# Kernel tuning notes

Measured on AMD Instinct MI355X. Metric: run time of the kernel, lower is better.

Reference implementation:

```python
import jax, jax.numpy as jnp
import numpy as np

B, T, C = 256, 2048, 64  # batch, max_seq_len, num_classes


def setup_inputs() -> dict:
    key = jax.random.key(0)
    k1, k2, k3, k4 = jax.random.split(key, 4)
    pad_x = jax.random.normal(k1, (B, T, C), dtype=jnp.float32)
    transitions = jax.random.uniform(k2, (C, C), dtype=jnp.float32)
    origination = jax.random.uniform(k3, (C,), dtype=jnp.float32)
    batch_sizes = jnp.sort(jax.random.randint(k4, (B,), 1, T + 1))
    # the torch implementation assumes features are zero-padded past the length
    mask = jnp.arange(T)[None, :] < batch_sizes[:, None]  # (B, T)
    pad_x = pad_x * mask[:, :, None]
    return {"pad_x": pad_x, "transitions": transitions,
            "origination": origination, "batch_sizes": batch_sizes}


def reference(pad_x, transitions, origination, batch_sizes):
    # Linear-chain CRF forward algorithm (faithful to torch _forward_algo,
    # including the final sum over classes rather than logsumexp).
    x_tbc = jnp.swapaxes(pad_x, 0, 1)  # (T, B, C)
    alpha0 = x_tbc[0] + origination[None, :]  # (B, C)

    def step(alpha_prev, x_t):
        # scores[b, j, k] = alpha_prev[b, k] + transitions[j, k]
        scores = alpha_prev[:, None, :] + transitions[None, :, :]  # (B, C, C)
        alpha = x_t + jax.nn.logsumexp(scores, axis=2)  # (B, C)
        return alpha, alpha

    _, alphas_rest = jax.lax.scan(step, alpha0, x_tbc[1:])
    alphas = jnp.concatenate([alpha0[None], alphas_rest], axis=0)  # (T, B, C)
    # gather alpha at the last valid timestep of each sequence
    final = alphas[batch_sizes - 1, jnp.arange(pad_x.shape[0])]  # (B, C)
    return final.sum(axis=1)  # (B,)
```

## Files before the change

### kernel.cpp

```cpp
#include <hip/hip_runtime.h>


#define CC 64

typedef short bf16x8 __attribute__((ext_vector_type(8)));
typedef float f32x4 __attribute__((ext_vector_type(4)));

union PackAB { int w[4]; bf16x8 v; };

__device__ __forceinline__ int cvtpk(float lo, float hi) {
    int r;
    asm("v_cvt_pk_bf16_f32 %0, %1, %2" : "=v"(r) : "v"(lo), "v"(hi));
    return r;
}
__device__ __forceinline__ float bcast0(float v) {
    return __int_as_float(__builtin_amdgcn_readfirstlane(__float_as_int(v)));
}

#define LDS_FENCE() asm volatile("s_waitcnt lgkmcnt(0)" ::: "memory")

template <bool SCALE>
__device__ __forceinline__ void chain_step(const bf16x8 (&A)[4][2], PackAB (&Bf)[2][4],
                                           const f32x4* __restrict__ er4, int g,
                                           float r_, float& ns0) {
    f32x4 er[4];
    #pragma unroll
    for (int mt = 0; mt < 4; ++mt) {
        er[mt] = er4[4 * mt + g];
        if (SCALE) er[mt] *= r_;
    }

    f32x4 D[4][4];
    #pragma unroll
    for (int nt = 0; nt < 4; ++nt) {
        f32x4 Z = {0.f, 0.f, 0.f, 0.f};
        #pragma unroll
        for (int mt = 0; mt < 4; ++mt)
            D[nt][mt] = __builtin_amdgcn_mfma_f32_16x16x32_bf16(A[mt][0], Bf[0][nt].v, Z, 0, 0, 0);
    }
    #pragma unroll
    for (int nt = 0; nt < 4; ++nt)
        #pragma unroll
        for (int mt = 0; mt < 4; ++mt)
            D[nt][mt] = __builtin_amdgcn_mfma_f32_16x16x32_bf16(A[mt][1], Bf[1][nt].v, D[nt][mt], 0, 0, 0);

    ns0 = D[0][0][0];

    #pragma unroll
    for (int nt = 0; nt < 4; ++nt) {
        f32x4 d0 = D[nt][0] * er[0];
        f32x4 d1 = D[nt][1] * er[1];
        f32x4 d2 = D[nt][2] * er[2];
        f32x4 d3 = D[nt][3] * er[3];
        Bf[0][nt].w[0] = cvtpk(d0[0], d0[1]);
        Bf[0][nt].w[1] = cvtpk(d0[2], d0[3]);
        Bf[0][nt].w[2] = cvtpk(d1[0], d1[1]);
        Bf[0][nt].w[3] = cvtpk(d1[2], d1[3]);
        Bf[1][nt].w[0] = cvtpk(d2[0], d2[1]);
        Bf[1][nt].w[1] = cvtpk(d2[2], d2[3]);
        Bf[1][nt].w[2] = cvtpk(d3[0], d3[1]);
        Bf[1][nt].w[3] = cvtpk(d3[2], d3[3]);
    }

    __builtin_amdgcn_sched_group_barrier(0x100, 4, 0);
    __builtin_amdgcn_sched_group_barrier(0x008, 32, 0);
    __builtin_amdgcn_sched_group_barrier(0x002, 80, 0);
}

__launch_bounds__(64, 2)
__global__ void crf_seg_kernel(const float* __restrict__ x,
                               const float* __restrict__ trans,
                               const int*   __restrict__ lens,
                               unsigned short* __restrict__ Mws,
                               float* __restrict__ Ls,
                               int T, int Pseg, int SEG, int B) {
    const int blk = blockIdx.x;
    const int b = B - 1 - (blk >> 6);
    const int s = blk & (Pseg - 1);
    const int L = lens[b];
    const int tbeg = s * SEG;
    int segend = (s + 1) * SEG; if (segend > L - 1) segend = L - 1;
    const int nsteps = segend - tbeg;
    if (nsteps <= 0) return;

    const int l = threadIdx.x;
    const int c = l & 15, g = l >> 4;
    const float L2E = 1.4426950408889634f;
    const float* xb = x + (size_t)b * T * CC;

    __shared__ float xl[32][CC];

    {
        const int rl = l >> 4;
        const int cl = (l & 15) * 4;
        f32x4 st[8];
        #pragma unroll
        for (int i = 0; i < 8; ++i) {
            int tr = tbeg + 1 + 4 * i + rl;
            if (tr > segend) tr = segend;
            st[i] = *(const f32x4*)(xb + (size_t)tr * CC + cl);
        }
        #pragma unroll
        for (int i = 0; i < 8; ++i) {
            f32x4 e;
            #pragma unroll
            for (int r = 0; r < 4; ++r)
                e[r] = __builtin_amdgcn_exp2f(st[i][r] * L2E);
            *(f32x4*)&xl[4 * i + rl][cl] = e;
        }
        LDS_FENCE();
    }

    bf16x8 A[4][2];
    #pragma unroll
    for (int mt = 0; mt < 4; ++mt) {
        const float* tr = trans + (16 * mt + c) * CC;
        #pragma unroll
        for (int ch = 0; ch < 2; ++ch) {
            float4 u = *(const float4*)(tr + 32 * ch + 4 * g);
            float4 v = *(const float4*)(tr + 32 * ch + 16 + 4 * g);
            PackAB pk;
            pk.w[0] = cvtpk(__builtin_amdgcn_exp2f(u.x * L2E), __builtin_amdgcn_exp2f(u.y * L2E));
            pk.w[1] = cvtpk(__builtin_amdgcn_exp2f(u.z * L2E), __builtin_amdgcn_exp2f(u.w * L2E));
            pk.w[2] = cvtpk(__builtin_amdgcn_exp2f(v.x * L2E), __builtin_amdgcn_exp2f(v.y * L2E));
            pk.w[3] = cvtpk(__builtin_amdgcn_exp2f(v.z * L2E), __builtin_amdgcn_exp2f(v.w * L2E));
            A[mt][ch] = pk.v;
        }
    }
    PackAB Bf[2][4];
    #pragma unroll
    for (int ch = 0; ch < 2; ++ch)
        #pragma unroll
        for (int nt = 0; nt < 4; ++nt)
            #pragma unroll
            for (int qq = 0; qq < 4; ++qq) {
                int i0 = 2 * qq, i1 = 2 * qq + 1;
                int k0 = 32 * ch + 4 * g + (i0 & 3) + 16 * (i0 >> 2);
                int k1 = 32 * ch + 4 * g + (i1 & 3) + 16 * (i1 >> 2);
                Bf[ch][nt].w[qq] = cvtpk((k0 == 16 * nt + c) ? 1.f : 0.f,
                                         (k1 == 16 * nt + c) ? 1.f : 0.f);
            }

    float Lseg = 0.f, ns0 = 1.0f;
    for (int base = 0; base < nsteps; base += 4) {
        float r_ = 1.0f;
        if (base > 0) {
            float S00 = bcast0(ns0);
            r_ = __builtin_amdgcn_rcpf(S00);
            Lseg -= __builtin_amdgcn_logf(r_);
        }
        chain_step<true >(A, Bf, (const f32x4*)&xl[base][0], g, r_, ns0);
        if (base + 1 < nsteps) chain_step<false>(A, Bf, (const f32x4*)&xl[base + 1][0], g, 1.f, ns0);
        if (base + 2 < nsteps) chain_step<false>(A, Bf, (const f32x4*)&xl[base + 2][0], g, 1.f, ns0);
        if (base + 3 < nsteps) chain_step<false>(A, Bf, (const f32x4*)&xl[base + 3][0], g, 1.f, ns0);
    }

    unsigned short* Mo = Mws + ((size_t)b * Pseg + s) * 4096;
    #pragma unroll
    for (int ch = 0; ch < 2; ++ch)
        #pragma unroll
        for (int nt = 0; nt < 4; ++nt)
            #pragma unroll
            for (int e = 0; e < 8; ++e) {
                unsigned wb = (unsigned)Bf[ch][nt].w[e >> 1];
                unsigned short hb = (e & 1) ? (unsigned short)(wb >> 16)
                                            : (unsigned short)(wb & 0xffffu);
                int row = 32 * ch + 4 * g + (e & 3) + 16 * (e >> 2);
                Mo[row * 64 + 16 * nt + c] = hb;
            }
    if (l == 0) Ls[(size_t)b * Pseg + s] = Lseg;
}

__launch_bounds__(64, 1)
__global__ void crf_apply_kernel(const float* __restrict__ x,
                                 const float* __restrict__ orig,
                                 const int*   __restrict__ lens,
                                 const unsigned short* __restrict__ Mws,
                                 const float* __restrict__ Ls,
                                 float* __restrict__ out,
                                 int T, int Pseg, int SEG) {
    const int b = blockIdx.x, j = threadIdx.x;
    __shared__ float qb[CC];
    const float L2E = 1.4426950408889634f, LN2 = 0.6931471805599453f;
    const int L = lens[b];
    const float* xb = x + (size_t)b * T * CC;

    float Mbar = (xb[0] + orig[0]) * L2E;
    float q = __builtin_amdgcn_exp2f((xb[j] + orig[j]) * L2E - Mbar);

    uint4 R[8];
    {
        const uint4* Ms = (const uint4*)(Mws + ((size_t)b * Pseg + 0) * 4096 + j * 64);
        #pragma unroll
        for (int i = 0; i < 8; ++i) R[i] = Ms[i];
    }

    for (int s = 0; s < Pseg; ++s) {
        int tbeg = s * SEG;
        int segend = (s + 1) * SEG; if (segend > L - 1) segend = L - 1;
        if (segend - tbeg <= 0) break;

        uint4 Rc[8];
        #pragma unroll
        for (int i = 0; i < 8; ++i) Rc[i] = R[i];
        {
            int s2 = (s + 1 < Pseg) ? s + 1 : s;
            const uint4* Ms = (const uint4*)(Mws + ((size_t)b * Pseg + s2) * 4096 + j * 64);
            #pragma unroll
            for (int i = 0; i < 8; ++i) R[i] = Ms[i];
        }

        qb[j] = q;
        LDS_FENCE();

        float acc = 0.f;
        #pragma unroll
        for (int i = 0; i < 8; ++i) {
            f32x4 qv0 = *(const f32x4*)&qb[8 * i];
            f32x4 qv1 = *(const f32x4*)&qb[8 * i + 4];
            unsigned u0 = Rc[i].x, u1 = Rc[i].y, u2 = Rc[i].z, u3 = Rc[i].w;
            acc = fmaf(__uint_as_float(u0 << 16),        qv0[0], acc);
            acc = fmaf(__uint_as_float(u0 & 0xffff0000), qv0[1], acc);
            acc = fmaf(__uint_as_float(u1 << 16),        qv0[2], acc);
            acc = fmaf(__uint_as_float(u1 & 0xffff0000), qv0[3], acc);
            acc = fmaf(__uint_as_float(u2 << 16),        qv1[0], acc);
            acc = fmaf(__uint_as_float(u2 & 0xffff0000), qv1[1], acc);
            acc = fmaf(__uint_as_float(u3 << 16),        qv1[2], acc);
            acc = fmaf(__uint_as_float(u3 & 0xffff0000), qv1[3], acc);
        }
        float S = acc;
        Mbar += Ls[(size_t)b * Pseg + s];
        float p = bcast0(S);
        float r = __builtin_amdgcn_rcpf(p);
        float lgr = __builtin_amdgcn_logf(r);
        q = S * r;
        Mbar -= lgr;
        LDS_FENCE();
    }

    float alpha = LN2 * (Mbar + __builtin_amdgcn_logf(q));
    alpha += __shfl_xor(alpha, 1, 64);
    alpha += __shfl_xor(alpha, 2, 64);
    alpha += __shfl_xor(alpha, 4, 64);
    alpha += __shfl_xor(alpha, 8, 64);
    alpha += __shfl_xor(alpha, 16, 64);
    alpha += __shfl_xor(alpha, 32, 64);
    if (j == 0) out[b] = alpha;
}

extern "C" void kernel_launch(void* const* d_in, const int* in_sizes, int n_in,
                              void* d_out, int out_size, void* d_ws, size_t ws_size,
                              hipStream_t stream) {
    const float* x     = (const float*)d_in[0];
    const float* trans = (const float*)d_in[1];
    const float* orig  = (const float*)d_in[2];
    const int*   lens  = (const int*)d_in[3];
    float* out = (float*)d_out;

    const int B = in_sizes[3];
    const int T = in_sizes[0] / (B * CC);

    const int P = 64;
    const int SEG = (T + P - 1) / P;

    unsigned short* Mws = (unsigned short*)d_ws;
    float* Ls = (float*)(Mws + (size_t)B * P * 4096);

    crf_seg_kernel<<<B * P, 64, 0, stream>>>(x, trans, lens, Mws, Ls,
                                             T, P, SEG, B);
    crf_apply_kernel<<<B, 64, 0, stream>>>(x, orig, lens, Mws, Ls, out, T, P, SEG);
}
```

Before: 182.4 us.

## Split segment chain into two interleaved halves and merge via matrix product

Each wave's segment of transfer-matrix products is split into two independent 16-step sub-chains that run interleaved, giving the MFMA pipeline two independent dependency chains to overlap. The second half's product is staged through LDS, reloaded as an A operand, multiplied with the first half's result, then renormalized and packed back. This trades a longer serial MFMA dependency chain for extra registers, one more 64x64 matrix multiply, and an LDS round trip. It assumes the segment is at most 32 steps.

```diff
diff --git a/kernel.cpp b/kernel.cpp
--- a/kernel.cpp
+++ b/kernel.cpp
@@ -127,7 +127,7 @@
             A[mt][ch] = pk.v;
         }
     }
-    PackAB Bf[2][4];
+    PackAB Bf0[2][4], Bf1[2][4];
     #pragma unroll
     for (int ch = 0; ch < 2; ++ch)
         #pragma unroll
@@ -137,22 +137,99 @@
                 int i0 = 2 * qq, i1 = 2 * qq + 1;
                 int k0 = 32 * ch + 4 * g + (i0 & 3) + 16 * (i0 >> 2);
                 int k1 = 32 * ch + 4 * g + (i1 & 3) + 16 * (i1 >> 2);
-                Bf[ch][nt].w[qq] = cvtpk((k0 == 16 * nt + c) ? 1.f : 0.f,
-                                         (k1 == 16 * nt + c) ? 1.f : 0.f);
+                int idv = cvtpk((k0 == 16 * nt + c) ? 1.f : 0.f,
+                                (k1 == 16 * nt + c) ? 1.f : 0.f);
+                Bf0[ch][nt].w[qq] = idv;
+                Bf1[ch][nt].w[qq] = idv;
             }
 
-    float Lseg = 0.f, ns0 = 1.0f;
-    for (int base = 0; base < nsteps; base += 4) {
-        float r_ = 1.0f;
-        if (base > 0) {
-            float S00 = bcast0(ns0);
-            r_ = __builtin_amdgcn_rcpf(S00);
-            Lseg -= __builtin_amdgcn_logf(r_);
-        }
-        chain_step<true >(A, Bf, (const f32x4*)&xl[base][0], g, r_, ns0);
-        if (base + 1 < nsteps) chain_step<false>(A, Bf, (const f32x4*)&xl[base + 1][0], g, 1.f, ns0);
-        if (base + 2 < nsteps) chain_step<false>(A, Bf, (const f32x4*)&xl[base + 2][0], g, 1.f, ns0);
-        if (base + 3 < nsteps) chain_step<false>(A, Bf, (const f32x4*)&xl[base + 3][0], g, 1.f, ns0);
+    const int n0 = nsteps < 16 ? nsteps : 16;
+    int n1 = nsteps - 16; if (n1 < 0) n1 = 0;
+
+    float Ls0 = 0.f, ns00 = 1.0f;
+    float Ls1 = 0.f, ns01 = 1.0f;
+
+    for (int base = 0; base < 16; base += 4) {
+        float r0 = 1.0f, r1 = 1.0f;
+        if (base > 0 && base < n0) {
+            float S00 = bcast0(ns00);
+            r0 = __builtin_amdgcn_rcpf(S00);
+            Ls0 -= __builtin_amdgcn_logf(r0);
+        }
+        if (base > 0 && base < n1) {
+            float S01 = bcast0(ns01);
+            r1 = __builtin_amdgcn_rcpf(S01);
+            Ls1 -= __builtin_amdgcn_logf(r1);
+        }
+        if (base     < n0) chain_step<true >(A, Bf0, (const f32x4*)&xl[base][0],      g, r0,  ns00);
+        if (base     < n1) chain_step<true >(A, Bf1, (const f32x4*)&xl[16 + base][0], g, r1,  ns01);
+        if (base + 1 < n0) chain_step<false>(A, Bf0, (const f32x4*)&xl[base + 1][0],  g, 1.f, ns00);
+        if (base + 1 < n1) chain_step<false>(A, Bf1, (const f32x4*)&xl[16 + base + 1][0], g, 1.f, ns01);
+        if (base + 2 < n0) chain_step<false>(A, Bf0, (const f32x4*)&xl[base + 2][0],  g, 1.f, ns00);
+        if (base + 2 < n1) chain_step<false>(A, Bf1, (const f32x4*)&xl[16 + base + 2][0], g, 1.f, ns01);
+        if (base + 3 < n0) chain_step<false>(A, Bf0, (const f32x4*)&xl[base + 3][0],  g, 1.f, ns00);
+        if (base + 3 < n1) chain_step<false>(A, Bf1, (const f32x4*)&xl[16 + base + 3][0], g, 1.f, ns01);
+    }
+
+    float Lfinal = Ls0;
+    if (n1 > 0) {
+        unsigned short* Ml = (unsigned short*)&xl[0][0];
+        LDS_FENCE();
+        #pragma unroll
+        for (int ch = 0; ch < 2; ++ch)
+            #pragma unroll
+            for (int nt = 0; nt < 4; ++nt)
+                #pragma unroll
+                for (int e = 0; e < 8; ++e) {
+                    unsigned wb = (unsigned)Bf1[ch][nt].w[e >> 1];
+                    unsigned short hb = (e & 1) ? (unsigned short)(wb >> 16)
+                                                : (unsigned short)(wb & 0xffffu);
+                    int row = 32 * ch + 4 * g + (e & 3) + 16 * (e >> 2);
+                    Ml[row * 64 + 16 * nt + c] = hb;
+                }
+        LDS_FENCE();
+        bf16x8 Ah[4][2];
+        #pragma unroll
+        for (int mt = 0; mt < 4; ++mt)
+            #pragma unroll
+            for (int ch = 0; ch < 2; ++ch) {
+                PackAB pk;
+                *(uint2*)&pk.w[0] = *(const uint2*)(Ml + (16 * mt + c) * 64 + 32 * ch + 4 * g);
+                *(uint2*)&pk.w[2] = *(const uint2*)(Ml + (16 * mt + c) * 64 + 32 * ch + 16 + 4 * g);
+                Ah[mt][ch] = pk.v;
+            }
+        f32x4 D[4][4];
+        #pragma unroll
+        for (int nt = 0; nt < 4; ++nt) {
+            f32x4 Z = {0.f, 0.f, 0.f, 0.f};
+            #pragma unroll
+            for (int mt = 0; mt < 4; ++mt)
+                D[nt][mt] = __builtin_amdgcn_mfma_f32_16x16x32_bf16(Ah[mt][0], Bf0[0][nt].v, Z, 0, 0, 0);
+        }
+        #pragma unroll
+        for (int nt = 0; nt < 4; ++nt)
+            #pragma unroll
+            for (int mt = 0; mt < 4; ++mt)
+                D[nt][mt] = __builtin_amdgcn_mfma_f32_16x16x32_bf16(Ah[mt][1], Bf0[1][nt].v, D[nt][mt], 0, 0, 0);
+
+        float S00 = bcast0(D[0][0][0]);
+        float r_  = __builtin_amdgcn_rcpf(S00);
+        Lfinal = Ls0 + Ls1 - __builtin_amdgcn_logf(r_);
+        #pragma unroll
+        for (int nt = 0; nt < 4; ++nt) {
+            f32x4 d0 = D[nt][0] * r_;
+            f32x4 d1 = D[nt][1] * r_;
+            f32x4 d2 = D[nt][2] * r_;
+            f32x4 d3 = D[nt][3] * r_;
+            Bf0[0][nt].w[0] = cvtpk(d0[0], d0[1]);
+            Bf0[0][nt].w[1] = cvtpk(d0[2], d0[3]);
+            Bf0[0][nt].w[2] = cvtpk(d1[0], d1[1]);
+            Bf0[0][nt].w[3] = cvtpk(d1[2], d1[3]);
+            Bf0[1][nt].w[0] = cvtpk(d2[0], d2[1]);
+            Bf0[1][nt].w[1] = cvtpk(d2[2], d2[3]);
+            Bf0[1][nt].w[2] = cvtpk(d3[0], d3[1]);
+            Bf0[1][nt].w[3] = cvtpk(d3[2], d3[3]);
+        }
     }
 
     unsigned short* Mo = Mws + ((size_t)b * Pseg + s) * 4096;
@@ -162,13 +239,13 @@
         for (int nt = 0; nt < 4; ++nt)
             #pragma unroll
             for (int e = 0; e < 8; ++e) {
-                unsigned wb = (unsigned)Bf[ch][nt].w[e >> 1];
+                unsigned wb = (unsigned)Bf0[ch][nt].w[e >> 1];
                 unsigned short hb = (e & 1) ? (unsigned short)(wb >> 16)
                                             : (unsigned short)(wb & 0xffffu);
                 int row = 32 * ch + 4 * g + (e & 3) + 16 * (e >> 2);
                 Mo[row * 64 + 16 * nt + c] = hb;
             }
-    if (l == 0) Ls[(size_t)b * Pseg + s] = Lseg;
+    if (l == 0) Ls[(size_t)b * Pseg + s] = Lfinal;
 }
 
 __launch_bounds__(64, 1)
```

Result: slower. 197.0 us (+8.0%).
